# Kernel tuning notes

Hardware: AMD Instinct MI355X
Metric: run time of the kernel (lower is better)

## Reference

```python
import jax, jax.numpy as jnp
import numpy as np

B, T, D, H = 4, 2048, 1024, 16
DK = D // H


def setup_inputs() -> dict:
    key = jax.random.key(0)
    ks = jax.random.split(key, 8)
    s = 0.02
    return {
        "query": jax.random.normal(ks[0], (B, T, D), jnp.float32),
        "key": jax.random.normal(ks[1], (B, T, D), jnp.float32),
        "value": jax.random.normal(ks[2], (B, T, D), jnp.float32),
        "mask": jnp.ones((B, T, T), jnp.int32),  # 1 = attend, 0 = masked out
        "Wq": jax.random.normal(ks[3], (D, D), jnp.float32) * s,
        "bq": jnp.zeros((D,), jnp.float32),
        "Wk": jax.random.normal(ks[4], (D, D), jnp.float32) * s,
        "bk": jnp.zeros((D,), jnp.float32),
        "Wv": jax.random.normal(ks[5], (D, D), jnp.float32) * s,
        "bv": jnp.zeros((D,), jnp.float32),
        "Wo": jax.random.normal(ks[6], (D, D), jnp.float32) * s,
        "bo": jnp.zeros((D,), jnp.float32),
    }


def reference(query, key, value, mask, Wq, bq, Wk, bk, Wv, bv, Wo, bo):
    b, t1, d = query.shape
    h, dk = H, DK
    # linear projections (torch nn.Linear: x @ W.T + b), split heads
    q = (query @ Wq.T + bq).reshape(b, t1, h, dk).transpose(0, 2, 1, 3)  # b h t1 dk
    k = (key @ Wk.T + bk).reshape(b, -1, h, dk).transpose(0, 2, 1, 3)    # b h t2 dk
    v = (value @ Wv.T + bv).reshape(b, -1, h, dk).transpose(0, 2, 1, 3)  # b h t2 dk
    scores = jnp.einsum('bhqd,bhkd->bhqk', q, k) / jnp.sqrt(jnp.float32(dk))
    neg = jnp.finfo(scores.dtype).min
    m = (mask[:, None, :, :] == 0)  # b 1 t1 t2 broadcast over heads
    scores = jnp.where(m, neg, scores)
    attn = jax.nn.softmax(scores, axis=-1)
    attn = jnp.where(m, 0.0, attn)
    # dropout_rate = 0.0 -> identity
    x = jnp.einsum('bhqk,bhkd->bhqd', attn, v)
    x = x.transpose(0, 2, 1, 3).reshape(b, t1, h * dk)
    out = x @ Wo.T + bo
    return out, attn
```

## Files before the change

kernel.cpp:

```cpp
#include <hip/hip_runtime.h>
#include <hip/hip_bf16.h>
#include <stdint.h>

#define B_ 4
#define T_ 2048
#define D_ 1024
#define H_ 16
#define DK_ 64
#define LOG2E 1.44269504088896340736f
#define NEGF (-3.0e38f)

typedef __attribute__((ext_vector_type(8))) short bf16x8;
typedef __attribute__((ext_vector_type(4))) float f32x4;

#define FENCE()   asm volatile("" ::: "memory")
#define SCHEDB()  __builtin_amdgcn_sched_barrier(0)
#define SBAR()    __builtin_amdgcn_s_barrier()
#define WAITV0()  asm volatile("s_waitcnt vmcnt(0)" ::: "memory")
#define WAITV2()  asm volatile("s_waitcnt vmcnt(2)" ::: "memory")
#define WAITV4()  asm volatile("s_waitcnt vmcnt(4)" ::: "memory")
#define WAITV6()  asm volatile("s_waitcnt vmcnt(6)" ::: "memory")
#define WAITL0()  asm volatile("s_waitcnt lgkmcnt(0)" ::: "memory")
#define WAITLV4() asm volatile("s_waitcnt lgkmcnt(0) vmcnt(4)" ::: "memory")

__device__ inline unsigned short f2bf(float f){
  union { __hip_bfloat16 h; unsigned short u; } v;
  v.h = __hip_bfloat16(f);
  return v.u;
}
__device__ inline unsigned int pk2(float a, float b){
  return (unsigned int)f2bf(a) | ((unsigned int)f2bf(b) << 16);
}
__device__ inline float fexp2(float x){ return __builtin_amdgcn_exp2f(x); }
__device__ inline f32x4 mfma16(bf16x8 a, bf16x8 b, f32x4 c){
  return __builtin_amdgcn_mfma_f32_16x16x32_bf16(a, b, c, 0, 0, 0);
}
__device__ inline bf16x8 lds_frag(const unsigned short* base, int row, int slot){
  return *(const bf16x8*)((const char*)base + row*128 + ((slot ^ (row & 7)) << 4));
}
__device__ inline void gload16(const void* g, void* l){
  __builtin_amdgcn_global_load_lds((const __attribute__((address_space(1))) void*)g,
                                   (__attribute__((address_space(3))) void*)l, 16, 0, 0);
}
__device__ inline void stage_gl128(const unsigned short* __restrict__ g, int ld,
                                   unsigned short* lds, int wave, int lane){
#pragma unroll
  for (int i = 0; i < 4; ++i){
    int row = wave*32 + i*8 + (lane >> 3);
    int c = (lane & 7) ^ (row & 7);
    gload16(g + (size_t)row*ld + c*8, lds + (wave*32 + i*8)*64);
  }
}
__device__ inline void stage_gl64(const unsigned short* __restrict__ g, int ld,
                                  unsigned short* lds, int wave, int lane){
#pragma unroll
  for (int i = 0; i < 2; ++i){
    int row = wave*16 + i*8 + (lane >> 3);
    int c = (lane & 7) ^ (row & 7);
    gload16(g + (size_t)row*ld + c*8, lds + (wave*16 + i*8)*64);
  }
}

__global__ void pack_mask_k(const int* __restrict__ mask, unsigned long long* __restrict__ bits){
  int i = blockIdx.x * 256 + threadIdx.x;
  unsigned long long b = __ballot(mask[i] != 0);
  if ((threadIdx.x & 63) == 0) bits[i >> 6] = b;
}

__global__ void convall_k(const float* __restrict__ Wq, const float* __restrict__ Wk,
                          const float* __restrict__ Wv, const float* __restrict__ Wo,
                          const float* __restrict__ q, const float* __restrict__ k,
                          const float* __restrict__ v,
                          unsigned short* __restrict__ wdst, unsigned short* __restrict__ xdst){
  int g = blockIdx.x*256 + threadIdx.x;
  const float* s; unsigned short* d; int off;
  if (g < 524288){
    int w = g >> 17; off = (g & 131071) * 8;
    s = (w==0) ? Wq : (w==1) ? Wk : (w==2) ? Wv : Wo;
    d = wdst + (size_t)w*1048576 + off;
  } else {
    int gg = g - 524288;
    int w = gg >> 20; off = (gg & 1048575) * 8;
    s = (w==0) ? q : (w==1) ? k : v;
    d = xdst + (size_t)w*8388608 + off;
  }
  float4 a = *(const float4*)(s + off);
  float4 b2 = *(const float4*)(s + off + 4);
  uint4 o;
  o.x = pk2(a.x,a.y); o.y = pk2(a.z,a.w); o.z = pk2(b2.x,b2.y); o.w = pk2(b2.z,b2.w);
  *(uint4*)d = o;
}

__global__ __launch_bounds__(256, 3)
void gemm_in(const unsigned short* __restrict__ Xbf, const unsigned short* __restrict__ Wbf,
             const float* __restrict__ bq, const float* __restrict__ bk,
             const float* __restrict__ bv,
             unsigned short* __restrict__ QKout, unsigned short* __restrict__ Vt)
{
  __shared__ __align__(16) unsigned short As[128*64];
  __shared__ __align__(16) unsigned short Bs[128*64];
  const int tid = threadIdx.x, lane = tid & 63, wave = tid >> 6;
  const int lcol = lane & 15, lgrp = lane >> 4;
  const int id = blockIdx.x;
  const bool vmode = (id >= 1024);
  int mtile, ntile;
  const unsigned short *A, *W;
  if (!vmode){
    int z = id >> 9, rem = id & 511;
    mtile = rem >> 3; ntile = rem & 7;
    A = Xbf + (size_t)z*8388608;
    W = Wbf + (size_t)z*1048576;
  } else {
    int rem = id - 1024;
    mtile = rem >> 6; ntile = rem & 63;
    A = Wbf + (size_t)2*1048576;
    W = Xbf + (size_t)2*8388608;
  }
  const int wm = (wave & 1) * 64, wn = (wave >> 1) * 64;
  f32x4 acc[4][4] = {};
#pragma unroll 1
  for (int kt = 0; kt < 16; ++kt){
    stage_gl128(A + (size_t)(mtile*128)*1024 + kt*64, 1024, As, wave, lane);
    stage_gl128(W + (size_t)(ntile*128)*1024 + kt*64, 1024, Bs, wave, lane);
    __syncthreads();
    bf16x8 af[4][2], bfr[4][2];
#pragma unroll
    for (int mi=0;mi<4;mi++)
#pragma unroll
      for (int kh=0;kh<2;kh++)
        af[mi][kh] = lds_frag(As, wm + mi*16 + lcol, kh*4 + lgrp);
#pragma unroll
    for (int ni=0;ni<4;ni++)
#pragma unroll
      for (int kh=0;kh<2;kh++)
        bfr[ni][kh] = lds_frag(Bs, wn + ni*16 + lcol, kh*4 + lgrp);
    __builtin_amdgcn_s_setprio(1);
#pragma unroll
    for (int mi=0;mi<4;mi++)
#pragma unroll
      for (int ni=0;ni<4;ni++)
#pragma unroll
        for (int kh=0;kh<2;kh++)
          acc[mi][ni] = mfma16(af[mi][kh], bfr[ni][kh], acc[mi][ni]);
    __builtin_amdgcn_s_setprio(0);
    __syncthreads();
  }
  if (!vmode){
    int z = id >> 9;
    const float* bias = z ? bk : bq;
    unsigned short* C = QKout + (size_t)z*8388608;
    float osc = z ? 1.0f : 0.125f*LOG2E;
#pragma unroll
    for (int mi=0;mi<4;mi++)
#pragma unroll
      for (int ni=0;ni<4;ni++){
        int n = ntile*128 + wn + ni*16 + lcol;
#pragma unroll
        for (int r=0;r<4;r++){
          int m = mtile*128 + wm + mi*16 + lgrp*4 + r;
          float v = (acc[mi][ni][r] + bias[n]) * osc;
          int bb = m >> 11, t = m & 2047, hh = n >> 6, dk = n & 63;
          C[(((size_t)(bb*H_ + hh)*T_ + t) << 6) + dk] = f2bf(v);
        }
      }
  } else {
#pragma unroll
    for (int mi=0;mi<4;mi++)
#pragma unroll
      for (int ni=0;ni<4;ni++){
        int n = ntile*128 + wn + ni*16 + lcol;
#pragma unroll
        for (int r=0;r<4;r++){
          int m = mtile*128 + wm + mi*16 + lgrp*4 + r;
          float v = acc[mi][ni][r] + bv[m];
          int bb = n >> 11, t = n & 2047, hh = m >> 6, dk = m & 63;
          Vt[(((size_t)(bb*H_ + hh)*DK_ + dk) << 11) + t] = f2bf(v);
        }
      }
  }
}

__global__ __launch_bounds__(256, 3)
void gemm_out(const unsigned short* __restrict__ A, const unsigned short* __restrict__ W,
              const float* __restrict__ bias, float* __restrict__ C)
{
  __shared__ __align__(16) unsigned short As[128*64];
  __shared__ __align__(16) unsigned short Bs[128*64];
  const int tid = threadIdx.x, lane = tid & 63, wave = tid >> 6;
  const int lcol = lane & 15, lgrp = lane >> 4;
  const int mtile = blockIdx.y, ntile = blockIdx.x;
  const int wm = (wave & 1) * 64, wn = (wave >> 1) * 64;
  f32x4 acc[4][4] = {};
#pragma unroll 1
  for (int kt = 0; kt < 16; ++kt){
    int m0 = mtile*128; int b = m0 >> 11; int t0 = m0 & 2047;
    const unsigned short* xbase = A + (((size_t)(b*16 + kt)*2048 + t0) << 6);
    stage_gl128(xbase, 64, As, wave, lane);
    stage_gl128(W + (size_t)(ntile*128)*1024 + kt*64, 1024, Bs, wave, lane);
    __syncthreads();
    bf16x8 af[4][2], bfr[4][2];
#pragma unroll
    for (int mi=0;mi<4;mi++)
#pragma unroll
      for (int kh=0;kh<2;kh++)
        af[mi][kh] = lds_frag(As, wm + mi*16 + lcol, kh*4 + lgrp);
#pragma unroll
    for (int ni=0;ni<4;ni++)
#pragma unroll
      for (int kh=0;kh<2;kh++)
        bfr[ni][kh] = lds_frag(Bs, wn + ni*16 + lcol, kh*4 + lgrp);
    __builtin_amdgcn_s_setprio(1);
#pragma unroll
    for (int mi=0;mi<4;mi++)
#pragma unroll
      for (int ni=0;ni<4;ni++)
#pragma unroll
        for (int kh=0;kh<2;kh++)
          acc[mi][ni] = mfma16(af[mi][kh], bfr[ni][kh], acc[mi][ni]);
    __builtin_amdgcn_s_setprio(0);
    __syncthreads();
  }
#pragma unroll
  for (int mi=0;mi<4;mi++)
#pragma unroll
    for (int ni=0;ni<4;ni++){
      int n = ntile*128 + wn + ni*16 + lcol;
#pragma unroll
      for (int r=0;r<4;r++){
        int m = mtile*128 + wm + mi*16 + lgrp*4 + r;
        C[(size_t)m*D_ + n] = acc[mi][ni][r] + bias[n];
      }
    }
}

__global__ __launch_bounds__(256, 4)
void attn_k(const unsigned short* __restrict__ Qbh, const unsigned short* __restrict__ Kbh,
            const unsigned short* __restrict__ Vt, const unsigned long long* __restrict__ mbits,
            float* __restrict__ attn, unsigned short* __restrict__ Xq)
{
  __shared__ __align__(16) unsigned short KV[4][64*64];
  __shared__ __align__(16) unsigned short Ps[64*64];
  const int tid = threadIdx.x, lane = tid & 63, wave = tid >> 6;
  const int lcol = lane & 15, lgrp = lane >> 4;
  const int id = blockIdx.x;
  const int sub = id >> 3;
  const int bh = (id & 7)*8 + (sub >> 5);
  const int qt = sub & 31;
  const int b = bh >> 4;
  const int q0 = qt * 64;

  const unsigned short* Kbase = Kbh + ((size_t)bh*T_) * DK_;
  const unsigned short* Vbase = Vt + (size_t)bh*DK_*T_;

  bool mall;
  {
    int* flag = (int*)Ps;
    const ulonglong2* mp = (const ulonglong2*)(mbits + ((size_t)b*T_ + q0)*32) + tid*4;
    unsigned long long macc = ~0ull;
#pragma unroll
    for (int i=0;i<4;i++){ ulonglong2 v = mp[i]; macc &= v.x & v.y; }
    if (tid == 0) *flag = 1;
    __syncthreads();
    if (!__all(macc == ~0ull) && (lane == 0)) atomicAnd(flag, 0);
    __syncthreads();
    mall = (*flag != 0);
    WAITL0();
  }

  stage_gl64(Qbh + ((size_t)bh*T_ + q0)*DK_, 64, Ps, wave, lane);
  stage_gl64(Kbase,             64, KV[0], wave, lane);
  stage_gl64(Kbase + 64*DK_,    64, KV[1], wave, lane);
  stage_gl64(Kbase + 2*64*DK_,  64, KV[2], wave, lane);
  __syncthreads();
  bf16x8 qf[2];
#pragma unroll
  for (int kh=0;kh<2;kh++) qf[kh] = lds_frag(Ps, wave*16 + lcol, kh*4 + lgrp);

  const int qr = wave*16 + lcol;
  const unsigned long long* mrp = mbits + ((size_t)b*T_ + q0 + qr)*32;
  const int bit0 = lgrp*4;

  float lsum = 0.f;

  if (mall){
#pragma unroll 1
    for (int kv=0; kv<29; ++kv){
      stage_gl64(Kbase + (size_t)(kv+3)*64*DK_, 64, KV[(kv+3)&3], wave, lane);
      WAITV6(); SCHEDB(); SBAR();
      const unsigned short* kcur = KV[kv&3];
      f32x4 sf[4] = {};
      __builtin_amdgcn_s_setprio(1);
#pragma unroll
      for (int kh=0;kh<2;kh++)
#pragma unroll
        for (int kb=0;kb<4;kb++)
          sf[kb] = mfma16(lds_frag(kcur, kb*16 + lcol, kh*4 + lgrp), qf[kh], sf[kb]);
      __builtin_amdgcn_s_setprio(0);
      float part = 0.f;
#pragma unroll
      for (int kb=0;kb<4;kb++)
#pragma unroll
        for (int r=0;r<4;r++) part += fexp2(sf[kb][r]);
      lsum += part;
      WAITL0(); SCHEDB(); SBAR();
    }
#pragma unroll 1
    for (int kv=29; kv<32; ++kv){
      if (kv == 29) { WAITV4(); } else if (kv == 30) { WAITV2(); } else { WAITV0(); }
      SCHEDB(); SBAR();
      const unsigned short* kcur = KV[kv&3];
      f32x4 sf[4] = {};
      __builtin_amdgcn_s_setprio(1);
#pragma unroll
      for (int kh=0;kh<2;kh++)
#pragma unroll
        for (int kb=0;kb<4;kb++)
          sf[kb] = mfma16(lds_frag(kcur, kb*16 + lcol, kh*4 + lgrp), qf[kh], sf[kb]);
      __builtin_amdgcn_s_setprio(0);
      float part = 0.f;
#pragma unroll
      for (int kb=0;kb<4;kb++)
#pragma unroll
        for (int r=0;r<4;r++) part += fexp2(sf[kb][r]);
      lsum += part;
      WAITL0(); SCHEDB(); SBAR();
    }
  } else {
#pragma unroll 1
    for (int kv=0; kv<32; ++kv){
      if (kv < 31) stage_gl64(Kbase + (size_t)(kv+1)*64*DK_, 64, KV[(kv+1)&1], wave, lane);
      const unsigned short* kcur = KV[kv&1];
      f32x4 sf[4] = {};
#pragma unroll
      for (int kh=0;kh<2;kh++)
#pragma unroll
        for (int kb=0;kb<4;kb++)
          sf[kb] = mfma16(lds_frag(kcur, kb*16 + lcol, kh*4 + lgrp), qf[kh], sf[kb]);
      unsigned long long w = mrp[kv];
      float part = 0.f;
#pragma unroll
      for (int kb=0;kb<4;kb++)
#pragma unroll
        for (int r=0;r<4;r++)
          part += fexp2(((w >> (kb*16 + bit0 + r)) & 1ull) ? sf[kb][r] : NEGF);
      lsum += part;
      __syncthreads();
    }
  }

  lsum += __shfl_xor(lsum, 16);
  lsum += __shfl_xor(lsum, 32);
  const float mmr = (lsum > 0.f) ? __log2f(lsum) : 3.0e38f;

  f32x4 oacc[4] = {};
  float* abase = attn + ((size_t)bh*T_ + q0)*T_;

  unsigned short* const Ks0 = KV[0];
  unsigned short* const Ks1 = KV[1];
  unsigned short* const Vt0 = KV[2];
  unsigned short* const Vt1 = KV[3];
  stage_gl64(Kbase, 64, Ks0, wave, lane);
  stage_gl64(Vbase, T_, Vt0, wave, lane);

  if (mall){
    WAITV0(); SCHEDB(); SBAR();
#pragma unroll 1
    for (int kv=0; kv<32; ++kv){
      if (kv < 31){
        stage_gl64(Kbase + (size_t)(kv+1)*64*DK_, 64, (kv&1) ? Ks0 : Ks1, wave, lane);
        stage_gl64(Vbase + (size_t)(kv+1)*64, T_, (kv&1) ? Vt0 : Vt1, wave, lane);
      }
      FENCE(); SCHEDB();
      const unsigned short* kcur = (kv&1) ? Ks1 : Ks0;
      f32x4 sf[4] = {};
      __builtin_amdgcn_s_setprio(1);
#pragma unroll
      for (int kh=0;kh<2;kh++)
#pragma unroll
        for (int kb=0;kb<4;kb++)
          sf[kb] = mfma16(lds_frag(kcur, kb*16 + lcol, kh*4 + lgrp), qf[kh], sf[kb]);
      __builtin_amdgcn_s_setprio(0);
      float* arow = abase + (size_t)qr*T_ + kv*64 + bit0;
      char* prow = (char*)Ps + qr*128 + ((lgrp & 1) << 3);
      const int sw = qr & 7;
#pragma unroll
      for (int kb=0;kb<4;kb++){
        float p0 = fexp2(sf[kb][0] - mmr);
        float p1 = fexp2(sf[kb][1] - mmr);
        float p2 = fexp2(sf[kb][2] - mmr);
        float p3 = fexp2(sf[kb][3] - mmr);
        f32x4 st = {p0, p1, p2, p3};
        __builtin_nontemporal_store(st, (f32x4*)(arow + kb*16));
        uint2 pb;
        pb.x = pk2(p0, p1);
        pb.y = pk2(p2, p3);
        *(uint2*)(prow + ((((kb << 1) | (lgrp >> 1)) ^ sw) << 4)) = pb;
      }
      WAITL0(); SCHEDB(); SBAR();
      const unsigned short* vcur = (kv&1) ? Vt1 : Vt0;
      __builtin_amdgcn_s_setprio(1);
#pragma unroll
      for (int kh=0;kh<2;kh++){
        bf16x8 af = lds_frag(vcur, wave*16 + lcol, kh*4 + lgrp);
#pragma unroll
        for (int qb=0;qb<4;qb++)
          oacc[qb] = mfma16(af, lds_frag(Ps, qb*16 + lcol, kh*4 + lgrp), oacc[qb]);
      }
      __builtin_amdgcn_s_setprio(0);
      WAITLV4(); SCHEDB(); SBAR();
    }
  } else {
    __syncthreads();
#pragma unroll 1
    for (int kv=0; kv<32; ++kv){
      if (kv < 31){
        stage_gl64(Kbase + (size_t)(kv+1)*64*DK_, 64, (kv&1) ? Ks0 : Ks1, wave, lane);
        stage_gl64(Vbase + (size_t)(kv+1)*64, T_, (kv&1) ? Vt0 : Vt1, wave, lane);
      }
      unsigned long long w = mrp[kv];
      const unsigned short* kcur = (kv&1) ? Ks1 : Ks0;
      f32x4 sf[4] = {};
#pragma unroll
      for (int kh=0;kh<2;kh++)
#pragma unroll
        for (int kb=0;kb<4;kb++)
          sf[kb] = mfma16(lds_frag(kcur, kb*16 + lcol, kh*4 + lgrp), qf[kh], sf[kb]);
      float* arow = abase + (size_t)qr*T_ + kv*64 + bit0;
      char* prow = (char*)Ps + qr*128 + ((lgrp & 1) << 3);
      const int sw = qr & 7;
#pragma unroll
      for (int kb=0;kb<4;kb++){
        float p0 = fexp2(sf[kb][0] - mmr);
        float p1 = fexp2(sf[kb][1] - mmr);
        float p2 = fexp2(sf[kb][2] - mmr);
        float p3 = fexp2(sf[kb][3] - mmr);
        p0 = ((w >> (kb*16 + bit0    )) & 1ull) ? p0 : 0.f;
        p1 = ((w >> (kb*16 + bit0 + 1)) & 1ull) ? p1 : 0.f;
        p2 = ((w >> (kb*16 + bit0 + 2)) & 1ull) ? p2 : 0.f;
        p3 = ((w >> (kb*16 + bit0 + 3)) & 1ull) ? p3 : 0.f;
        f32x4 st = {p0, p1, p2, p3};
        __builtin_nontemporal_store(st, (f32x4*)(arow + kb*16));
        uint2 pb;
        pb.x = pk2(p0, p1);
        pb.y = pk2(p2, p3);
        *(uint2*)(prow + ((((kb << 1) | (lgrp >> 1)) ^ sw) << 4)) = pb;
      }
      __syncthreads();
      const unsigned short* vcur = (kv&1) ? Vt1 : Vt0;
#pragma unroll
      for (int kh=0;kh<2;kh++){
        bf16x8 af = lds_frag(vcur, wave*16 + lcol, kh*4 + lgrp);
#pragma unroll
        for (int qb=0;qb<4;qb++)
          oacc[qb] = mfma16(af, lds_frag(Ps, qb*16 + lcol, kh*4 + lgrp), oacc[qb]);
      }
      __syncthreads();
    }
  }

  unsigned short* Es = KV[0];
#pragma unroll
  for (int qb=0;qb<4;qb++){
    uint2 pv;
    pv.x = pk2(oacc[qb][0], oacc[qb][1]);
    pv.y = pk2(oacc[qb][2], oacc[qb][3]);
    *(uint2*)(Es + (qb*16 + lcol)*68 + wave*16 + lgrp*4) = pv;
  }
  __syncthreads();
  unsigned short* xrow = Xq + ((size_t)bh*T_ + q0)*DK_;
#pragma unroll
  for (int it=0; it<4; ++it){
    int idx = tid + it*256;
    int q = idx >> 4, sl = idx & 15;
    uint2 v = *(const uint2*)(Es + q*68 + sl*4);
    *(uint2*)(xrow + (size_t)q*64 + sl*4) = v;
  }
}

extern "C" void kernel_launch(void* const* d_in, const int* in_sizes, int n_in,
                              void* d_out, int out_size, void* d_ws, size_t ws_size,
                              hipStream_t stream) {
  const float* query = (const float*)d_in[0];
  const float* key   = (const float*)d_in[1];
  const float* value = (const float*)d_in[2];
  const int*   mask  = (const int*)d_in[3];
  const float* Wq = (const float*)d_in[4];  const float* bq = (const float*)d_in[5];
  const float* Wk = (const float*)d_in[6];  const float* bk = (const float*)d_in[7];
  const float* Wv = (const float*)d_in[8];  const float* bv = (const float*)d_in[9];
  const float* Wo = (const float*)d_in[10]; const float* bo = (const float*)d_in[11];

  float* out  = (float*)d_out;
  float* attn = out + (size_t)B_*T_*D_;

  char* ws = (char*)d_ws;
  unsigned short* Qbh = (unsigned short*)(ws);
  unsigned short* Kbh = (unsigned short*)(ws + ((size_t)16<<20));
  unsigned short* Vt  = (unsigned short*)(ws + ((size_t)32<<20));
  unsigned long long* mb = (unsigned long long*)(ws + ((size_t)48<<20));
  unsigned short* Wbf = (unsigned short*)(ws + ((size_t)50<<20));
  unsigned short* Xbf = (unsigned short*)attn;

  pack_mask_k<<<dim3((B_*T_*T_)/256), 256, 0, stream>>>(mask, mb);
  convall_k<<<dim3(14336), 256, 0, stream>>>(Wq, Wk, Wv, Wo, query, key, value, Wbf, Xbf);
  gemm_in<<<dim3(1536), 256, 0, stream>>>(Xbf, Wbf, bq, bk, bv, Qbh, Vt);
  attn_k<<<dim3(2048), 256, 0, stream>>>(Qbh, Kbh, Vt, mb, attn, Qbh);
  gemm_out<<<dim3(8,64), 256, 0, stream>>>(Qbh, Wbf + (3u<<20), bo, out);
}
```

Measured before the change: 464.0 us.

## Load Q and K fragments directly from global memory in softmax-sum pass

The first (row-sum) pass of attention now reads Q and K MFMA fragments straight from global memory into registers. This replaces the LDS staging with its 4-deep ring buffer, waitcnts and barriers, and the loop is unrolled by 2 so the compiler can overlap loads. The goal is to remove barrier and LDS round-trip overhead, since every wave reads its own fragments and nothing is shared. The cost is that each wave issues its own global loads of K, which may be redundant across the 4 waves and rely on L1/L2 hits, and latency hiding now depends on compiler scheduling.

```diff
diff --git a/kernel.cpp b/kernel.cpp
--- a/kernel.cpp
+++ b/kernel.cpp
@@ -17,9 +17,6 @@
 #define SCHEDB()  __builtin_amdgcn_sched_barrier(0)
 #define SBAR()    __builtin_amdgcn_s_barrier()
 #define WAITV0()  asm volatile("s_waitcnt vmcnt(0)" ::: "memory")
-#define WAITV2()  asm volatile("s_waitcnt vmcnt(2)" ::: "memory")
-#define WAITV4()  asm volatile("s_waitcnt vmcnt(4)" ::: "memory")
-#define WAITV6()  asm volatile("s_waitcnt vmcnt(6)" ::: "memory")
 #define WAITL0()  asm volatile("s_waitcnt lgkmcnt(0)" ::: "memory")
 #define WAITLV4() asm volatile("s_waitcnt lgkmcnt(0) vmcnt(4)" ::: "memory")
 
@@ -267,75 +264,59 @@
     WAITL0();
   }
 
-  stage_gl64(Qbh + ((size_t)bh*T_ + q0)*DK_, 64, Ps, wave, lane);
-  stage_gl64(Kbase,             64, KV[0], wave, lane);
-  stage_gl64(Kbase + 64*DK_,    64, KV[1], wave, lane);
-  stage_gl64(Kbase + 2*64*DK_,  64, KV[2], wave, lane);
-  __syncthreads();
+  const int qr = wave*16 + lcol;
   bf16x8 qf[2];
-#pragma unroll
-  for (int kh=0;kh<2;kh++) qf[kh] = lds_frag(Ps, wave*16 + lcol, kh*4 + lgrp);
-
-  const int qr = wave*16 + lcol;
+  {
+    const unsigned short* qrow = Qbh + ((size_t)bh*T_ + q0 + qr)*DK_ + lgrp*8;
+    qf[0] = *(const bf16x8*)(qrow);
+    qf[1] = *(const bf16x8*)(qrow + 32);
+  }
+
   const unsigned long long* mrp = mbits + ((size_t)b*T_ + q0 + qr)*32;
   const int bit0 = lgrp*4;
 
   float lsum = 0.f;
 
+  const unsigned short* kp0 = Kbase + (size_t)lcol*DK_ + lgrp*8;
   if (mall){
-#pragma unroll 1
-    for (int kv=0; kv<29; ++kv){
-      stage_gl64(Kbase + (size_t)(kv+3)*64*DK_, 64, KV[(kv+3)&3], wave, lane);
-      WAITV6(); SCHEDB(); SBAR();
-      const unsigned short* kcur = KV[kv&3];
+#pragma unroll 2
+    for (int kv=0; kv<32; ++kv){
+      const unsigned short* kp = kp0 + (size_t)kv*64*DK_;
+      bf16x8 kf[2][4];
+#pragma unroll
+      for (int kh=0;kh<2;kh++)
+#pragma unroll
+        for (int kb=0;kb<4;kb++)
+          kf[kh][kb] = *(const bf16x8*)(kp + kb*16*DK_ + kh*32);
       f32x4 sf[4] = {};
-      __builtin_amdgcn_s_setprio(1);
-#pragma unroll
-      for (int kh=0;kh<2;kh++)
-#pragma unroll
-        for (int kb=0;kb<4;kb++)
-          sf[kb] = mfma16(lds_frag(kcur, kb*16 + lcol, kh*4 + lgrp), qf[kh], sf[kb]);
-      __builtin_amdgcn_s_setprio(0);
+#pragma unroll
+      for (int kh=0;kh<2;kh++)
+#pragma unroll
+        for (int kb=0;kb<4;kb++)
+          sf[kb] = mfma16(kf[kh][kb], qf[kh], sf[kb]);
       float part = 0.f;
 #pragma unroll
       for (int kb=0;kb<4;kb++)
 #pragma unroll
         for (int r=0;r<4;r++) part += fexp2(sf[kb][r]);
       lsum += part;
-      WAITL0(); SCHEDB(); SBAR();
-    }
-#pragma unroll 1
-    for (int kv=29; kv<32; ++kv){
-      if (kv == 29) { WAITV4(); } else if (kv == 30) { WAITV2(); } else { WAITV0(); }
-      SCHEDB(); SBAR();
-      const unsigned short* kcur = KV[kv&3];
-      f32x4 sf[4] = {};
-      __builtin_amdgcn_s_setprio(1);
-#pragma unroll
-      for (int kh=0;kh<2;kh++)
-#pragma unroll
-        for (int kb=0;kb<4;kb++)
-          sf[kb] = mfma16(lds_frag(kcur, kb*16 + lcol, kh*4 + lgrp), qf[kh], sf[kb]);
-      __builtin_amdgcn_s_setprio(0);
-      float part = 0.f;
-#pragma unroll
-      for (int kb=0;kb<4;kb++)
-#pragma unroll
-        for (int r=0;r<4;r++) part += fexp2(sf[kb][r]);
-      lsum += part;
-      WAITL0(); SCHEDB(); SBAR();
     }
   } else {
-#pragma unroll 1
+#pragma unroll 2
     for (int kv=0; kv<32; ++kv){
-      if (kv < 31) stage_gl64(Kbase + (size_t)(kv+1)*64*DK_, 64, KV[(kv+1)&1], wave, lane);
-      const unsigned short* kcur = KV[kv&1];
+      const unsigned short* kp = kp0 + (size_t)kv*64*DK_;
+      bf16x8 kf[2][4];
+#pragma unroll
+      for (int kh=0;kh<2;kh++)
+#pragma unroll
+        for (int kb=0;kb<4;kb++)
+          kf[kh][kb] = *(const bf16x8*)(kp + kb*16*DK_ + kh*32);
       f32x4 sf[4] = {};
 #pragma unroll
       for (int kh=0;kh<2;kh++)
 #pragma unroll
         for (int kb=0;kb<4;kb++)
-          sf[kb] = mfma16(lds_frag(kcur, kb*16 + lcol, kh*4 + lgrp), qf[kh], sf[kb]);
+          sf[kb] = mfma16(kf[kh][kb], qf[kh], sf[kb]);
       unsigned long long w = mrp[kv];
       float part = 0.f;
 #pragma unroll
@@ -344,7 +325,6 @@
         for (int r=0;r<4;r++)
           part += fexp2(((w >> (kb*16 + bit0 + r)) & 1ull) ? sf[kb][r] : NEGF);
       lsum += part;
-      __syncthreads();
     }
   }
 
```

Result: slower. 514.0 us (+10.8%).
